# Performance work log

Measured on AMD Instinct MI355X. Metric: run time of the kernel, lower is better.

The kernel has to match this reference:

```python
import jax, jax.numpy as jnp
import numpy as np

TILE = 16            # TILE_WIDTH == TILE_HEIGHT in the Taichi kernel
H, W = 512, 512
TV, TU = H // TILE, W // TILE
NT = TV * TU         # number of 16x16 tiles
PPT = 64             # depth-sorted points assigned to each tile (uniform/padded)
N = NT * PPT


def setup_inputs() -> dict:
    key = jax.random.key(0)
    ks = jax.random.split(key, 7)
    # each tile owns a contiguous depth-sorted chunk of the global point list
    tile_of_point = jnp.arange(N) // PPT
    tu = (tile_of_point % TU).astype(jnp.float32)
    tv = (tile_of_point // TU).astype(jnp.float32)
    center = jnp.stack([tu * TILE + TILE / 2, tv * TILE + TILE / 2], -1)
    point_uv = center + jax.random.normal(ks[0], (N, 2)) * 6.0
    # conic = inverse 2x2 covariance packed as [a, b, c]; keep positive definite
    a = jax.random.uniform(ks[1], (N,), minval=0.02, maxval=0.3)
    c = jax.random.uniform(ks[2], (N,), minval=0.02, maxval=0.3)
    b = jax.random.uniform(ks[3], (N,), minval=-0.5, maxval=0.5) * jnp.sqrt(a * c)
    point_uv_conic = jnp.stack([a, b, c], -1)
    point_alpha_after_activation = jax.random.uniform(ks[4], (N,))
    point_color = jax.random.uniform(ks[5], (N, 3))
    # depths sorted within each tile chunk (front-to-back order, as after radix sort)
    point_depth = jnp.sort(
        jax.random.uniform(ks[6], (N,), minval=0.5, maxval=50.0).reshape(NT, PPT), axis=-1
    ).reshape(N)
    tile_point_indices = jnp.arange(N, dtype=jnp.int32).reshape(NT, PPT)
    return dict(point_uv=point_uv, point_uv_conic=point_uv_conic,
                point_alpha_after_activation=point_alpha_after_activation,
                point_color=point_color, point_depth=point_depth,
                tile_point_indices=tile_point_indices,
                camera_height=H, camera_width=W)


def _to_image(x, tv, tu):
    # x: [NT, TILE*TILE, ...] -> [H, W, ...] (tiles row-major, pixels row-major in tile)
    rest = x.shape[2:]
    x = x.reshape(tv, tu, TILE, TILE, *rest)
    x = jnp.swapaxes(x, 1, 2)
    return x.reshape(tv * TILE, tu * TILE, *rest)


def reference(point_uv, point_uv_conic, point_alpha_after_activation, point_color,
              point_depth, tile_point_indices, camera_height, camera_width):
    TU_ = camera_width // TILE
    TV_ = camera_height // TILE
    NT_ = TU_ * TV_
    PPT_ = tile_point_indices.shape[1]
    # gather per-tile point attributes: [NT, PPT, ...]
    g_uv = point_uv[tile_point_indices]
    g_conic = point_uv_conic[tile_point_indices]
    g_alpha = point_alpha_after_activation[tile_point_indices]
    g_color = point_color[tile_point_indices]
    g_depth = point_depth[tile_point_indices]
    # pixel centers for every tile: [NT, 256]
    p = jnp.arange(TILE * TILE)
    tid = jnp.arange(NT_)
    pix_u = (tid % TU_)[:, None].astype(jnp.float32) * TILE + (p % TILE).astype(jnp.float32)[None, :] + 0.5
    pix_v = (tid // TU_)[:, None].astype(jnp.float32) * TILE + (p // TILE).astype(jnp.float32)[None, :] + 0.5
    # Gaussian density from conic: exp(-0.5*(a dx^2 + c dy^2) - b dx dy)  [NT, 256, PPT]
    dx = pix_u[:, :, None] - g_uv[:, None, :, 0]
    dy = pix_v[:, :, None] - g_uv[:, None, :, 1]
    ca = g_conic[:, None, :, 0]; cb = g_conic[:, None, :, 1]; cc = g_conic[:, None, :, 2]
    dens = jnp.exp(-0.5 * (ca * dx * dx + cc * dy * dy) - cb * dx * dy)
    alpha = dens * g_alpha[:, None, :]
    visible = alpha >= 1.0 / 255.0           # kernel: continue if alpha < 1/255
    alpha_c = jnp.where(visible, jnp.minimum(alpha, 0.99), 0.0)
    one_m = 1.0 - alpha_c
    cp = jnp.cumprod(one_m, axis=-1)
    Ti = jnp.concatenate([jnp.ones_like(cp[..., :1]), cp[..., :-1]], axis=-1)  # exclusive transmittance
    # point whose next_T < 1e-4 saturates the pixel and is itself skipped
    trigger = visible & (Ti * one_m < 1e-4)
    saturated = jnp.cumsum(trigger.astype(jnp.int32), axis=-1) > 0
    contributes = visible & ~saturated
    w = jnp.where(contributes, alpha_c * Ti, 0.0)   # per-point compositing weight
    acc_color = jnp.einsum('tpk,tkc->tpc', w, g_color)
    norm = jnp.sum(w, axis=-1)
    acc_depth = jnp.sum(w * g_depth[:, None, :], axis=-1)
    T_final = jnp.prod(jnp.where(contributes, one_m, 1.0), axis=-1)
    valid_count = jnp.sum(contributes, axis=-1).astype(jnp.int32)
    j = jnp.arange(PPT_, dtype=jnp.int32)
    last = jnp.max(jnp.where(contributes, j[None, None, :] + 1, 0), axis=-1)
    last_offset = (jnp.arange(NT_, dtype=jnp.int32) * PPT_)[:, None] + last
    rasterized_image = _to_image(acc_color, TV_, TU_)
    rasterized_depth = _to_image(acc_depth / jnp.maximum(norm, 1e-6), TV_, TU_)
    pixel_accumulated_alpha = _to_image(1.0 - T_final, TV_, TU_)
    pixel_offset_of_last_effective_point = _to_image(last_offset, TV_, TU_)
    pixel_valid_point_count = _to_image(valid_count, TV_, TU_)
    return (rasterized_image, rasterized_depth, pixel_accumulated_alpha,
            pixel_offset_of_last_effective_point, pixel_valid_point_count)
```

## Files before the change

### kernel.cpp

```cpp
#include <hip/hip_runtime.h>
#include <hip/hip_fp16.h>

#define TILE 16
#define PPT 64

#if __has_builtin(__builtin_amdgcn_exp2f)
#define EXP2F(x) __builtin_amdgcn_exp2f(x)
#else
#define EXP2F(x) exp2f(x)
#endif

__device__ __forceinline__ int read_dim(const int* p) {
    int v = *p;
    if (v >= TILE && v <= 65536 && (v % TILE) == 0) return v;
    float f = __int_as_float(v);
    return (int)f;
}

__global__ __launch_bounds__(128, 2) void gsplat_raster_kernel(
    const float* __restrict__ point_uv,
    const float* __restrict__ point_conic,
    const float* __restrict__ point_alpha,
    const float* __restrict__ point_color,
    const float* __restrict__ point_depth,
    const int*   __restrict__ tile_point_indices,
    const int*   __restrict__ cam_h_p,
    const int*   __restrict__ cam_w_p,
    float* __restrict__ out)
{
    const int t = blockIdx.x;
    const int p = threadIdx.x;

    const int W  = read_dim(cam_w_p);
    const int H  = read_dim(cam_h_p);
    const int TU = W / TILE;
    const int n_pix = H * W;

    __shared__ float4 sA[PPT];
    __shared__ float4 sB[PPT];

    const float L2E = 1.4426950408889634f;
    if (p < PPT) {
        const int gi = tile_point_indices[t * PPT + p];
        const float2 uv = ((const float2*)point_uv)[gi];
        sA[p] = make_float4(uv.x, uv.y,
                            -0.5f * L2E * point_conic[gi * 3 + 0],
                            -0.5f * L2E * point_conic[gi * 3 + 2]);
    } else {
        const int q  = p - PPT;
        const int gi = tile_point_indices[t * PPT + q];
        const __half2 rg = __floats2half2_rn(point_color[gi * 3 + 0],
                                             point_color[gi * 3 + 1]);
        const __half2 bd = __floats2half2_rn(point_color[gi * 3 + 2],
                                             point_depth[gi]);
        sB[q] = make_float4(-L2E * point_conic[gi * 3 + 1],
                            __log2f(point_alpha[gi]),
                            __builtin_bit_cast(float, rg),
                            __builtin_bit_cast(float, bd));
    }
    __syncthreads();

    const int tu = t % TU;
    const int tv = t / TU;
    const int pu = p % TILE;
    const int pv0 = p / TILE;
    const int pv1 = pv0 + 8;
    const float pix_u  = (float)(tu * TILE + pu) + 0.5f;
    const float pix_v0 = (float)(tv * TILE + pv0) + 0.5f;
    const float pix_v1 = pix_v0 + 8.0f;

    float T0 = 1.0f, T1 = 1.0f;
    float r0 = 0.f, g0 = 0.f, b0 = 0.f, d0 = 0.f, n0 = 0.f;
    float r1 = 0.f, g1 = 0.f, b1 = 0.f, d1 = 0.f, n1 = 0.f;
    int cnt0 = 0, cnt1 = 0, last0 = 0, last1 = 0;
    bool sat0 = false, sat1 = false;

    for (int c8 = 0; c8 < PPT / 8; ++c8) {
        #pragma unroll
        for (int k = 0; k < 8; ++k) {
            const int j = c8 * 8 + k;
            const float4 A = sA[j];
            const float4 B = sB[j];

            const float dx   = pix_u - A.x;
            const float padx = A.z * dx;
            const __half2 rg = __builtin_bit_cast(__half2, B.z);
            const __half2 bd = __builtin_bit_cast(__half2, B.w);
            const float cr = __low2float(rg),  cg = __high2float(rg);
            const float cb = __low2float(bd),  cd = __high2float(bd);

            {
                const float dy = pix_v0 - A.y;
                const float e = fmaf(fmaf(B.x, dy, padx), dx,
                                     fmaf(A.w * dy, dy, B.y));
                const float alpha = EXP2F(e);
                const bool  vis     = alpha >= (1.0f / 255.0f);
                const float alpha_c = fminf(alpha, 0.99f);
                const float one_m   = 1.0f - alpha_c;
                const float Tone    = T0 * one_m;
                const bool  ntrig   = Tone >= 1e-4f;
                const bool  contrib = vis && ntrig && !sat0;
                sat0 = sat0 || (vis && !ntrig);
                const float w = contrib ? alpha_c * T0 : 0.0f;
                r0 = fmaf(w, cr, r0);  g0 = fmaf(w, cg, g0);
                b0 = fmaf(w, cb, b0);  d0 = fmaf(w, cd, d0);
                n0 += w;
                cnt0 += contrib;
                last0 = contrib ? j + 1 : last0;
                T0 = contrib ? Tone : T0;
            }
            {
                const float dy = pix_v1 - A.y;
                const float e = fmaf(fmaf(B.x, dy, padx), dx,
                                     fmaf(A.w * dy, dy, B.y));
                const float alpha = EXP2F(e);
                const bool  vis     = alpha >= (1.0f / 255.0f);
                const float alpha_c = fminf(alpha, 0.99f);
                const float one_m   = 1.0f - alpha_c;
                const float Tone    = T1 * one_m;
                const bool  ntrig   = Tone >= 1e-4f;
                const bool  contrib = vis && ntrig && !sat1;
                sat1 = sat1 || (vis && !ntrig);
                const float w = contrib ? alpha_c * T1 : 0.0f;
                r1 = fmaf(w, cr, r1);  g1 = fmaf(w, cg, g1);
                b1 = fmaf(w, cb, b1);  d1 = fmaf(w, cd, d1);
                n1 += w;
                cnt1 += contrib;
                last1 = contrib ? j + 1 : last1;
                T1 = contrib ? Tone : T1;
            }
        }
        if (__all(sat0 && sat1)) break;
    }

    const int c  = tu * TILE + pu;
    const int row0 = tv * TILE + pv0;
    const int pix0 = row0 * W + c;
    const int pix1 = pix0 + 8 * W;

    out[pix0 * 3 + 0] = r0;
    out[pix0 * 3 + 1] = g0;
    out[pix0 * 3 + 2] = b0;
    out[n_pix * 3 + pix0] = d0 / fmaxf(n0, 1e-6f);
    out[n_pix * 4 + pix0] = 1.0f - T0;
    out[n_pix * 5 + pix0] = (float)(t * PPT + last0);
    out[n_pix * 6 + pix0] = (float)cnt0;

    out[pix1 * 3 + 0] = r1;
    out[pix1 * 3 + 1] = g1;
    out[pix1 * 3 + 2] = b1;
    out[n_pix * 3 + pix1] = d1 / fmaxf(n1, 1e-6f);
    out[n_pix * 4 + pix1] = 1.0f - T1;
    out[n_pix * 5 + pix1] = (float)(t * PPT + last1);
    out[n_pix * 6 + pix1] = (float)cnt1;
}

extern "C" void kernel_launch(void* const* d_in, const int* in_sizes, int n_in,
                              void* d_out, int out_size, void* d_ws, size_t ws_size,
                              hipStream_t stream) {
    const float* point_uv    = (const float*)d_in[0];
    const float* point_conic = (const float*)d_in[1];
    const float* point_alpha = (const float*)d_in[2];
    const float* point_color = (const float*)d_in[3];
    const float* point_depth = (const float*)d_in[4];
    const int*   tpi         = (const int*)d_in[5];
    const int*   cam_h       = (const int*)d_in[6];
    const int*   cam_w       = (const int*)d_in[7];

    const int NT = in_sizes[5] / PPT;

    gsplat_raster_kernel<<<NT, 128, 0, stream>>>(
        point_uv, point_conic, point_alpha, point_color, point_depth,
        tpi, cam_h, cam_w, (float*)d_out);
}
```

Before: 20.04 us.

## Double-buffer shared-memory point loads and simplify per-pixel compositing math

Shared-memory point data is preloaded into registers in groups of four with a two-buffer software pipeline, so LDS reads for the next group overlap the compositing of the current one. The compositing step is reworked: visibility is tested in the log domain before the exp, the weight becomes T minus T times (1 minus alpha) so the separate norm accumulator goes away (norm is taken as 1 minus final T), and the saturation flag is folded into a gated transmittance. Colours and depth move from packed half to full fp32 in a separate shared array, which drops the conversions but uses more LDS and registers. The extra register buffers may reduce occupancy, and the reformulated norm and early-exit logic must match the reference's exact semantics.

```diff
diff --git a/kernel.cpp b/kernel.cpp
--- a/kernel.cpp
+++ b/kernel.cpp
@@ -1,8 +1,9 @@
 #include <hip/hip_runtime.h>
-#include <hip/hip_fp16.h>
 
 #define TILE 16
 #define PPT 64
+#define G 4
+#define NG (PPT / G)
 
 #if __has_builtin(__builtin_amdgcn_exp2f)
 #define EXP2F(x) __builtin_amdgcn_exp2f(x)
@@ -15,6 +16,27 @@
     if (v >= TILE && v <= 65536 && (v % TILE) == 0) return v;
     float f = __int_as_float(v);
     return (int)f;
+}
+
+__device__ __forceinline__ void composite(
+    float dy, float q, float base, float pcc,
+    float cr, float cg, float cb, float cd, int jp1,
+    float& T, float& Tg, float& ar, float& ag, float& ab, float& ad,
+    int& cnt, int& last)
+{
+    const float e     = fmaf(fmaf(pcc, dy, q), dy, base);
+    const bool  vis   = e >= -7.9943533f;
+    const float alpha = EXP2F(e);
+    const float one_m = fmaxf(1.0f - alpha, 0.01f);
+    const float Tone  = Tg * one_m;
+    const bool  contrib = vis && (Tone >= 1e-4f);
+    const float w = contrib ? (Tg - Tone) : 0.0f;
+    ar = fmaf(w, cr, ar);  ag = fmaf(w, cg, ag);
+    ab = fmaf(w, cb, ab);  ad = fmaf(w, cd, ad);
+    cnt += contrib;
+    last = contrib ? jp1 : last;
+    T  = contrib ? Tone : T;
+    Tg = vis ? (contrib ? Tone : 0.0f) : Tg;
 }
 
 __global__ __launch_bounds__(128, 2) void gsplat_raster_kernel(
@@ -37,7 +59,8 @@
     const int n_pix = H * W;
 
     __shared__ float4 sA[PPT];
-    __shared__ float4 sB[PPT];
+    __shared__ float2 sB[PPT];
+    __shared__ float4 sC[PPT];
 
     const float L2E = 1.4426950408889634f;
     if (p < PPT) {
@@ -46,111 +69,93 @@
         sA[p] = make_float4(uv.x, uv.y,
                             -0.5f * L2E * point_conic[gi * 3 + 0],
                             -0.5f * L2E * point_conic[gi * 3 + 2]);
+        sB[p] = make_float2(-L2E * point_conic[gi * 3 + 1],
+                            __log2f(point_alpha[gi]));
     } else {
         const int q  = p - PPT;
         const int gi = tile_point_indices[t * PPT + q];
-        const __half2 rg = __floats2half2_rn(point_color[gi * 3 + 0],
-                                             point_color[gi * 3 + 1]);
-        const __half2 bd = __floats2half2_rn(point_color[gi * 3 + 2],
-                                             point_depth[gi]);
-        sB[q] = make_float4(-L2E * point_conic[gi * 3 + 1],
-                            __log2f(point_alpha[gi]),
-                            __builtin_bit_cast(float, rg),
-                            __builtin_bit_cast(float, bd));
+        sC[q] = make_float4(point_color[gi * 3 + 0],
+                            point_color[gi * 3 + 1],
+                            point_color[gi * 3 + 2],
+                            point_depth[gi]);
     }
     __syncthreads();
 
-    const int tu = t % TU;
-    const int tv = t / TU;
-    const int pu = p % TILE;
+    const int tu  = t % TU;
+    const int tv  = t / TU;
+    const int pu  = p % TILE;
     const int pv0 = p / TILE;
-    const int pv1 = pv0 + 8;
     const float pix_u  = (float)(tu * TILE + pu) + 0.5f;
     const float pix_v0 = (float)(tv * TILE + pv0) + 0.5f;
-    const float pix_v1 = pix_v0 + 8.0f;
 
-    float T0 = 1.0f, T1 = 1.0f;
-    float r0 = 0.f, g0 = 0.f, b0 = 0.f, d0 = 0.f, n0 = 0.f;
-    float r1 = 0.f, g1 = 0.f, b1 = 0.f, d1 = 0.f, n1 = 0.f;
+    float T0 = 1.0f, T1 = 1.0f, Tg0 = 1.0f, Tg1 = 1.0f;
+    float r0 = 0.f, g0 = 0.f, b0 = 0.f, d0 = 0.f;
+    float r1 = 0.f, g1 = 0.f, b1 = 0.f, d1 = 0.f;
     int cnt0 = 0, cnt1 = 0, last0 = 0, last1 = 0;
-    bool sat0 = false, sat1 = false;
 
-    for (int c8 = 0; c8 < PPT / 8; ++c8) {
-        #pragma unroll
-        for (int k = 0; k < 8; ++k) {
-            const int j = c8 * 8 + k;
-            const float4 A = sA[j];
-            const float4 B = sB[j];
+    float4 A0[G], C0[G]; float2 B0[G];
+    float4 A1[G], C1[G]; float2 B1[G];
 
-            const float dx   = pix_u - A.x;
-            const float padx = A.z * dx;
-            const __half2 rg = __builtin_bit_cast(__half2, B.z);
-            const __half2 bd = __builtin_bit_cast(__half2, B.w);
-            const float cr = __low2float(rg),  cg = __high2float(rg);
-            const float cb = __low2float(bd),  cd = __high2float(bd);
+#define LOADG(BUF, g) do { const int _gb = (g) * G;                          \
+    _Pragma("unroll") for (int k = 0; k < G; ++k) {                          \
+        A##BUF[k] = sA[_gb + k];                                             \
+        B##BUF[k] = sB[_gb + k];                                             \
+        C##BUF[k] = sC[_gb + k];                                             \
+    } } while (0)
 
-            {
-                const float dy = pix_v0 - A.y;
-                const float e = fmaf(fmaf(B.x, dy, padx), dx,
-                                     fmaf(A.w * dy, dy, B.y));
-                const float alpha = EXP2F(e);
-                const bool  vis     = alpha >= (1.0f / 255.0f);
-                const float alpha_c = fminf(alpha, 0.99f);
-                const float one_m   = 1.0f - alpha_c;
-                const float Tone    = T0 * one_m;
-                const bool  ntrig   = Tone >= 1e-4f;
-                const bool  contrib = vis && ntrig && !sat0;
-                sat0 = sat0 || (vis && !ntrig);
-                const float w = contrib ? alpha_c * T0 : 0.0f;
-                r0 = fmaf(w, cr, r0);  g0 = fmaf(w, cg, g0);
-                b0 = fmaf(w, cb, b0);  d0 = fmaf(w, cd, d0);
-                n0 += w;
-                cnt0 += contrib;
-                last0 = contrib ? j + 1 : last0;
-                T0 = contrib ? Tone : T0;
-            }
-            {
-                const float dy = pix_v1 - A.y;
-                const float e = fmaf(fmaf(B.x, dy, padx), dx,
-                                     fmaf(A.w * dy, dy, B.y));
-                const float alpha = EXP2F(e);
-                const bool  vis     = alpha >= (1.0f / 255.0f);
-                const float alpha_c = fminf(alpha, 0.99f);
-                const float one_m   = 1.0f - alpha_c;
-                const float Tone    = T1 * one_m;
-                const bool  ntrig   = Tone >= 1e-4f;
-                const bool  contrib = vis && ntrig && !sat1;
-                sat1 = sat1 || (vis && !ntrig);
-                const float w = contrib ? alpha_c * T1 : 0.0f;
-                r1 = fmaf(w, cr, r1);  g1 = fmaf(w, cg, g1);
-                b1 = fmaf(w, cb, b1);  d1 = fmaf(w, cd, d1);
-                n1 += w;
-                cnt1 += contrib;
-                last1 = contrib ? j + 1 : last1;
-                T1 = contrib ? Tone : T1;
-            }
-        }
-        if (__all(sat0 && sat1)) break;
+#define COMPUTEG(BUF, g) do { const int _gb = (g) * G;                       \
+    _Pragma("unroll") for (int k = 0; k < G; ++k) {                          \
+        const float4 A = A##BUF[k];                                          \
+        const float2 B = B##BUF[k];                                          \
+        const float4 C = C##BUF[k];                                          \
+        const float dx   = pix_u - A.x;                                      \
+        const float q    = B.x * dx;                     \
+        const float base = fmaf(A.z * dx, dx, B.y);      \
+        const float dy0  = pix_v0 - A.y;                                     \
+        const float dy1  = dy0 + 8.0f;                                       \
+        const int   jp1  = _gb + k + 1;                                      \
+        composite(dy0, q, base, A.w, C.x, C.y, C.z, C.w, jp1,                \
+                  T0, Tg0, r0, g0, b0, d0, cnt0, last0);                     \
+        composite(dy1, q, base, A.w, C.x, C.y, C.z, C.w, jp1,                \
+                  T1, Tg1, r1, g1, b1, d1, cnt1, last1);                     \
+    } } while (0)
+
+    LOADG(0, 0);
+    #pragma unroll 1
+    for (int g = 0; g < NG; g += 2) {
+        LOADG(1, g + 1);
+        COMPUTEG(0, g);
+        if (__all((Tg0 == 0.0f) && (Tg1 == 0.0f))) break;
+        const int gn = (g + 2 < NG) ? g + 2 : NG - 1;
+        LOADG(0, gn);
+        COMPUTEG(1, g + 1);
+        if (__all((Tg0 == 0.0f) && (Tg1 == 0.0f))) break;
     }
 
-    const int c  = tu * TILE + pu;
+#undef LOADG
+#undef COMPUTEG
+
+    const int c    = tu * TILE + pu;
     const int row0 = tv * TILE + pv0;
     const int pix0 = row0 * W + c;
     const int pix1 = pix0 + 8 * W;
 
+    const float norm0 = 1.0f - T0;
+    const float norm1 = 1.0f - T1;
+
     out[pix0 * 3 + 0] = r0;
     out[pix0 * 3 + 1] = g0;
     out[pix0 * 3 + 2] = b0;
-    out[n_pix * 3 + pix0] = d0 / fmaxf(n0, 1e-6f);
-    out[n_pix * 4 + pix0] = 1.0f - T0;
+    out[n_pix * 3 + pix0] = d0 / fmaxf(norm0, 1e-6f);
+    out[n_pix * 4 + pix0] = norm0;
     out[n_pix * 5 + pix0] = (float)(t * PPT + last0);
     out[n_pix * 6 + pix0] = (float)cnt0;
 
     out[pix1 * 3 + 0] = r1;
     out[pix1 * 3 + 1] = g1;
     out[pix1 * 3 + 2] = b1;
-    out[n_pix * 3 + pix1] = d1 / fmaxf(n1, 1e-6f);
-    out[n_pix * 4 + pix1] = 1.0f - T1;
+    out[n_pix * 3 + pix1] = d1 / fmaxf(norm1, 1e-6f);
+    out[n_pix * 4 + pix1] = norm1;
     out[n_pix * 5 + pix1] = (float)(t * PPT + last1);
     out[n_pix * 6 + pix1] = (float)cnt1;
 }
```

Measured after the change: 20.30 us. Within noise of the previous version (+1.3%).
